# Performance work log

Hardware: AMD Instinct MI355X
Metric: run time of the kernel (lower is better)

Reference implementation:

```python
import jax, jax.numpy as jnp
import numpy as np

N = 100000
F_IN = 128
HID = 128
NCLS = 40
NEG_SLOPE = 0.2
BN_EPS = 1e-5


def setup_inputs() -> dict:
    key = jax.random.key(0)
    ks = jax.random.split(key, 16)
    x = jax.random.normal(ks[0], (N, F_IN), dtype=jnp.float32)
    # self-loop-free random edges: dst = (src + 1 + r) % N
    E = 1600000
    src = jax.random.randint(ks[1], (E,), 0, N)
    off = jax.random.randint(ks[2], (E,), 1, N)
    dst = (src + off) % N
    edge_index = jnp.stack([src, dst]).astype(jnp.int64)

    def glorot(k, shape):
        fan = shape[0] + shape[-1]
        s = jnp.sqrt(6.0 / fan)
        return jax.random.uniform(k, shape, jnp.float32, -s, s)

    params = {
        'W1': glorot(ks[3], (F_IN, HID)),
        'as1': glorot(ks[4], (HID,)), 'ad1': glorot(ks[5], (HID,)),
        'b1': jnp.zeros((HID,), jnp.float32),
        'g1': jnp.ones((HID,), jnp.float32), 'beta1': jnp.zeros((HID,), jnp.float32),
        'W2': glorot(ks[6], (HID, HID)),
        'as2': glorot(ks[7], (HID,)), 'ad2': glorot(ks[8], (HID,)),
        'b2': jnp.zeros((HID,), jnp.float32),
        'g2': jnp.ones((HID,), jnp.float32), 'beta2': jnp.zeros((HID,), jnp.float32),
        'Wc': glorot(ks[9], (HID, NCLS)),
        'bc': jnp.zeros((NCLS,), jnp.float32),
    }
    return {'x': x, 'edge_index': edge_index, **params}


def _gat_conv(h_in, src, dst, W, a_src, a_dst, bias):
    # heads=1, concat=False -> single head, mean over heads is identity
    h = h_in @ W                               # [N, C]
    alpha_s = h @ a_src                        # [N]
    alpha_d = h @ a_dst                        # [N]
    alpha = alpha_s[src] + alpha_d[dst]        # [E] edge score
    alpha = jax.nn.leaky_relu(alpha, NEG_SLOPE)
    # segment softmax over destination node neighborhoods
    m = jax.ops.segment_max(alpha, dst, num_segments=N)
    e = jnp.exp(alpha - m[dst])
    s = jax.ops.segment_sum(e, dst, num_segments=N)
    alpha = e / s[dst]
    msg = h[src] * alpha[:, None]              # [E, C]
    out = jax.ops.segment_sum(msg, dst, num_segments=N)
    return out + bias


def _batchnorm(x, gamma, beta):
    mu = jnp.mean(x, axis=0)
    var = jnp.mean(jnp.square(x - mu), axis=0)  # biased, as torch BN training
    return (x - mu) * jax.lax.rsqrt(var + BN_EPS) * gamma + beta


def reference(x, edge_index, W1, as1, ad1, b1, g1, beta1,
              W2, as2, ad2, b2, g2, beta2, Wc, bc):
    src, dst = edge_index[0], edge_index[1]
    # add self loops (input edges are guaranteed self-loop-free)
    loop = jnp.arange(N, dtype=src.dtype)
    src = jnp.concatenate([src, loop])
    dst = jnp.concatenate([dst, loop])

    h = _gat_conv(x, src, dst, W1, as1, ad1, b1)
    h = jax.nn.relu(_batchnorm(h, g1, beta1))
    h = _gat_conv(h, src, dst, W2, as2, ad2, b2)
    h = jax.nn.relu(_batchnorm(h, g2, beta2))
    return h @ Wc + bc
```

## Files before the change

### kernel.cpp

```cpp
#include <hip/hip_runtime.h>
#include <math.h>


#define CDIM 128
#define NCLS_ 40
#define NEG_SLOPE_ 0.2f
#define BN_EPS_ 1e-5f
#define BRNG 256
#define BCAP 6144
#define EPB 16

using short8  = __attribute__((ext_vector_type(8))) short;
using short4v = __attribute__((ext_vector_type(4))) short;
using f32x4   = __attribute__((ext_vector_type(4))) float;

static __device__ __forceinline__ float lrelu(float a) {
    return a > 0.f ? a : NEG_SLOPE_ * a;
}
static __device__ __forceinline__ short f2bf(float f) {
    unsigned u = __float_as_uint(f);
    u += 0x7fffu + ((u >> 16) & 1u);
    return (short)(u >> 16);
}
static __device__ __forceinline__ float bf_lo(unsigned u) { return __uint_as_float(u << 16); }
static __device__ __forceinline__ float bf_hi(unsigned u) { return __uint_as_float(u & 0xffff0000u); }

__global__ void k_setup(int* bcur, float* bnsum, int NB, int n, int E, int* offs,
                        const float* __restrict__ W1, const float* __restrict__ W2,
                        const float* __restrict__ Wc,
                        short* __restrict__ Wt1, short* __restrict__ Wt2,
                        short* __restrict__ Wtc) {
    int i = blockIdx.x * blockDim.x + threadIdx.x;
    if (i < NB) bcur[i] = 0;
    if (i < 512) bnsum[i] = 0.f;
    if (i == 0) offs[n] = E + n;
    if (i < 128 * 128) {
        int k = i >> 7, nn = i & 127;
        Wt1[nn * 128 + k] = f2bf(W1[i]);
        Wt2[nn * 128 + k] = f2bf(W2[i]);
    }
    if (i < 48 * 128) {
        int nn = i >> 7, k = i & 127;
        Wtc[i] = (nn < NCLS_) ? f2bf(Wc[k * NCLS_ + nn]) : (short)0;
    }
}

__global__ __launch_bounds__(256) void k_binA(
    const int* __restrict__ src, const int* __restrict__ dst, int E,
    int* __restrict__ bcur, uint2* __restrict__ bucket, int NB)
{
    __shared__ int hist[400];
    __shared__ int base[400];
    int t = threadIdx.x;
    long e0 = (long)blockIdx.x * (256 * EPB) + t;

    for (int i = t; i < NB; i += 256) hist[i] = 0;
    __syncthreads();

    int sv[EPB], dv[EPB];
    #pragma unroll
    for (int i = 0; i < EPB; i++) {
        long e = e0 + (long)i * 256;
        if (e < E) {
            sv[i] = src[e]; dv[i] = dst[e];
            atomicAdd(&hist[dv[i] >> 8], 1);
        } else dv[i] = -1;
    }
    __syncthreads();

    for (int i = t; i < NB; i += 256) {
        int h = hist[i];
        base[i] = (h > 0) ? atomicAdd(&bcur[i], h) : 0;
    }
    __syncthreads();
    for (int i = t; i < NB; i += 256) hist[i] = 0;
    __syncthreads();

    #pragma unroll
    for (int i = 0; i < EPB; i++) {
        if (dv[i] >= 0) {
            int b = dv[i] >> 8;
            int pos = base[b] + atomicAdd(&hist[b], 1);
            if (pos < BCAP)
                bucket[(size_t)b * BCAP + pos] =
                    make_uint2((unsigned)sv[i], (unsigned)dv[i]);
        }
    }
}

__global__ __launch_bounds__(256) void k_fillB(
    const uint2* __restrict__ bucket, const int* __restrict__ bcur,
    int n, int NB, int* __restrict__ offs, int* __restrict__ csr)
{
    __shared__ int hist[256];
    __shared__ int scanb[256];
    __shared__ int cur[256];
    __shared__ int buf[BCAP + BRNG];
    int b = blockIdx.x, t = threadIdx.x;
    int node0 = b << 8;
    int nodesIn = min(BRNG, n - node0);
    int cnt = min(bcur[b], BCAP);
    const uint2* mybkt = bucket + (size_t)b * BCAP;

    int part = 0;
    for (int j = t; j < b; j += 256) part += min(bcur[j], BCAP);
    scanb[t] = part; __syncthreads();
    for (int s2 = 128; s2 > 0; s2 >>= 1) {
        if (t < s2) scanb[t] += scanb[t + s2];
        __syncthreads();
    }
    int base = scanb[0] + node0;
    __syncthreads();

    hist[t] = 0; __syncthreads();
    for (int e2 = t; e2 < cnt; e2 += 256)
        atomicAdd(&hist[mybkt[e2].y & 255], 1);
    __syncthreads();

    int v = hist[t] + ((t < nodesIn) ? 1 : 0);
    scanb[t] = v; __syncthreads();
    for (int d = 1; d < 256; d <<= 1) {
        int x2 = (t >= d) ? scanb[t - d] : 0;
        __syncthreads();
        scanb[t] += x2;
        __syncthreads();
    }
    int lo = scanb[t] - v;
    if (t < nodesIn) {
        offs[node0 + t] = base + lo;
        buf[lo] = node0 + t;
        cur[t] = lo + 1;
    }
    __syncthreads();

    for (int e2 = t; e2 < cnt; e2 += 256) {
        uint2 ed = mybkt[e2];
        int pos = atomicAdd(&cur[ed.y & 255], 1);
        buf[pos] = (int)ed.x;
    }
    __syncthreads();

    int tot = cnt + nodesIn;
    for (int j2 = t; j2 < tot; j2 += 256) csr[base + j2] = buf[j2];
}

__global__ __launch_bounds__(256) void k_gemm_mfma(
    const float* __restrict__ Xf, const unsigned* __restrict__ Xb,
    const short* __restrict__ Wt,
    const float* __restrict__ bnsum, const float* __restrict__ gamma,
    const float* __restrict__ beta, float invn,
    const float* __restrict__ av_s, const float* __restrict__ av_d,
    short* __restrict__ Hb, float* __restrict__ alpha_s, float* __restrict__ alpha_d,
    int n, int fuse)
{
    __shared__ short As[64 * 128];
    __shared__ short Bs[128 * 128];
    __shared__ float part_s[4][64];
    __shared__ float part_d[4][64];
    int t = threadIdx.x;
    int row0 = blockIdx.x * 64;

    for (int j = 0; j < 8; j++) {
        int idx = j * 256 + t;
        int nn = idx >> 4, cc = idx & 15;
        *(short8*)(Bs + nn * 128 + cc * 8) = *(const short8*)(Wt + nn * 128 + cc * 8);
    }
    float4 sc4 = make_float4(1.f, 1.f, 1.f, 1.f);
    float4 sh4 = make_float4(0.f, 0.f, 0.f, 0.f);
    if (fuse) {
        int cb = (t & 31) * 4;
        float4 s0 = *(const float4*)(bnsum + cb);
        float4 s1 = *(const float4*)(bnsum + 128 + cb);
        float4 gm = *(const float4*)(gamma + cb);
        float4 bt = *(const float4*)(beta + cb);
        float mean, var;
        mean = s0.x * invn; var = fmaxf(s1.x * invn - mean * mean, 0.f);
        sc4.x = gm.x * rsqrtf(var + BN_EPS_); sh4.x = bt.x - mean * sc4.x;
        mean = s0.y * invn; var = fmaxf(s1.y * invn - mean * mean, 0.f);
        sc4.y = gm.y * rsqrtf(var + BN_EPS_); sh4.y = bt.y - mean * sc4.y;
        mean = s0.z * invn; var = fmaxf(s1.z * invn - mean * mean, 0.f);
        sc4.z = gm.z * rsqrtf(var + BN_EPS_); sh4.z = bt.z - mean * sc4.z;
        mean = s0.w * invn; var = fmaxf(s1.w * invn - mean * mean, 0.f);
        sc4.w = gm.w * rsqrtf(var + BN_EPS_); sh4.w = bt.w - mean * sc4.w;
    }
    for (int j = 0; j < 8; j++) {
        int idx = j * 256 + t;
        int r = idx >> 5, k4 = idx & 31;
        int gr = row0 + r;
        float4 xv = make_float4(0.f, 0.f, 0.f, 0.f);
        if (fuse) {
            if (gr < n) {
                uint2 u = *(const uint2*)(Xb + (size_t)gr * 64 + k4 * 2);
                xv.x = bf_lo(u.x); xv.y = bf_hi(u.x);
                xv.z = bf_lo(u.y); xv.w = bf_hi(u.y);
            }
            xv.x = fmaxf(fmaf(xv.x, sc4.x, sh4.x), 0.f);
            xv.y = fmaxf(fmaf(xv.y, sc4.y, sh4.y), 0.f);
            xv.z = fmaxf(fmaf(xv.z, sc4.z, sh4.z), 0.f);
            xv.w = fmaxf(fmaf(xv.w, sc4.w, sh4.w), 0.f);
        } else {
            if (gr < n) xv = *(const float4*)(Xf + (size_t)gr * CDIM + k4 * 4);
        }
        short4v o;
        o.x = f2bf(xv.x); o.y = f2bf(xv.y); o.z = f2bf(xv.z); o.w = f2bf(xv.w);
        *(short4v*)(As + r * 128 + k4 * 4) = o;
    }
    __syncthreads();

    int w = t >> 6, lane = t & 63, q = lane >> 4, c = lane & 15;
    f32x4 zero = {0.f, 0.f, 0.f, 0.f};
    f32x4 acc[4][2];
    for (int i = 0; i < 4; i++) { acc[i][0] = zero; acc[i][1] = zero; }

    for (int ks = 0; ks < 4; ks++) {
        int k0 = ks * 32 + q * 8;
        short8 a0 = *(short8*)(As + (c) * 128 + k0);
        short8 a1 = *(short8*)(As + (16 + c) * 128 + k0);
        short8 a2 = *(short8*)(As + (32 + c) * 128 + k0);
        short8 a3 = *(short8*)(As + (48 + c) * 128 + k0);
        short8 b0 = *(short8*)(Bs + (w * 32 + c) * 128 + k0);
        short8 b1 = *(short8*)(Bs + (w * 32 + 16 + c) * 128 + k0);
        acc[0][0] = __builtin_amdgcn_mfma_f32_16x16x32_bf16(a0, b0, acc[0][0], 0, 0, 0);
        acc[1][0] = __builtin_amdgcn_mfma_f32_16x16x32_bf16(a1, b0, acc[1][0], 0, 0, 0);
        acc[2][0] = __builtin_amdgcn_mfma_f32_16x16x32_bf16(a2, b0, acc[2][0], 0, 0, 0);
        acc[3][0] = __builtin_amdgcn_mfma_f32_16x16x32_bf16(a3, b0, acc[3][0], 0, 0, 0);
        acc[0][1] = __builtin_amdgcn_mfma_f32_16x16x32_bf16(a0, b1, acc[0][1], 0, 0, 0);
        acc[1][1] = __builtin_amdgcn_mfma_f32_16x16x32_bf16(a1, b1, acc[1][1], 0, 0, 0);
        acc[2][1] = __builtin_amdgcn_mfma_f32_16x16x32_bf16(a2, b1, acc[2][1], 0, 0, 0);
        acc[3][1] = __builtin_amdgcn_mfma_f32_16x16x32_bf16(a3, b1, acc[3][1], 0, 0, 0);
    }

    float as0 = av_s[w * 32 + c],      as1 = av_s[w * 32 + 16 + c];
    float ad0 = av_d[w * 32 + c],      ad1 = av_d[w * 32 + 16 + c];
    #pragma unroll
    for (int mt = 0; mt < 4; mt++) {
        #pragma unroll
        for (int r = 0; r < 4; r++) {
            float v0 = acc[mt][0][r], v1 = acc[mt][1][r];
            float ps = v0 * as0 + v1 * as1;
            float pd = v0 * ad0 + v1 * ad1;
            #pragma unroll
            for (int off = 1; off < 16; off <<= 1) {
                ps += __shfl_xor(ps, off);
                pd += __shfl_xor(pd, off);
            }
            if (c == 0) {
                part_s[w][mt * 16 + q * 4 + r] = ps;
                part_d[w][mt * 16 + q * 4 + r] = pd;
            }
        }
    }
    __syncthreads();

    short* Hs = As;
    #pragma unroll
    for (int mt = 0; mt < 4; mt++)
        #pragma unroll
        for (int nt = 0; nt < 2; nt++)
            #pragma unroll
            for (int r = 0; r < 4; r++)
                Hs[(mt * 16 + q * 4 + r) * 128 + w * 32 + nt * 16 + c] = f2bf(acc[mt][nt][r]);

    if (t < 64) {
        int row = row0 + t;
        if (row < n) {
            alpha_s[row] = part_s[0][t] + part_s[1][t] + part_s[2][t] + part_s[3][t];
            alpha_d[row] = part_d[0][t] + part_d[1][t] + part_d[2][t] + part_d[3][t];
        }
    }
    __syncthreads();

    for (int j = 0; j < 4; j++) {
        int idx = j * 256 + t;
        int r = idx >> 4, cc = idx & 15;
        int gr = row0 + r;
        if (gr < n)
            *(short8*)(Hb + (size_t)gr * 128 + cc * 8) = *(short8*)(Hs + r * 128 + cc * 8);
    }
}

__global__ __launch_bounds__(256) void k_agg(
    const uint2* __restrict__ Hb2, const int* __restrict__ offs,
    const int* __restrict__ csr, const float* __restrict__ alpha_s,
    const float* __restrict__ alpha_d, const float* __restrict__ bias,
    uint2* __restrict__ Ob, int n)
{
    int i = blockIdx.x * 8 + (threadIdx.x >> 5);
    int l = threadIdx.x & 31;
    if (i >= n) return;
    int o0 = offs[i], o1 = offs[i + 1];
    float adi = alpha_d[i];
    int hoff = (threadIdx.x & 32) << 2;

    float m = -1e30f, se = 0.f;
    float a0 = 0.f, a1 = 0.f, a2 = 0.f, a3 = 0.f;

    for (int c0 = o0; c0 < o1; c0 += 32) {
        int j = c0 + l;
        int cnt = min(32, o1 - c0);
        int sj = (j < o1) ? csr[j] : 0;
        float a = (j < o1) ? lrelu(alpha_s[sj] + adi) : -1e30f;

        float cm = a;
        #pragma unroll
        for (int o = 16; o > 0; o >>= 1) cm = fmaxf(cm, __shfl_xor(cm, o));
        if (cm > m) {
            float r = __expf(m - cm);
            se *= r; a0 *= r; a1 *= r; a2 *= r; a3 *= r;
            m = cm;
        }
        float wl = (j < o1) ? __expf(a - m) : 0.f;
        se += wl;
        int wli = (int)__float_as_uint(wl);

        int cntmax = max(cnt, __shfl_xor(cnt, 32));
        for (int b = 0; b < cntmax; b += 4) {
            uint2 u[4]; float wv[4];
            #pragma unroll
            for (int q2 = 0; q2 < 4; q2++) {
                int el = min(b + q2, 31);
                int addr = hoff + (el << 2);
                int s = __builtin_amdgcn_ds_bpermute(addr, sj);
                wv[q2] = __uint_as_float((unsigned)__builtin_amdgcn_ds_bpermute(addr, wli));
                u[q2] = Hb2[(size_t)(unsigned)s * 32 + l];
            }
            #pragma unroll
            for (int q2 = 0; q2 < 4; q2++) {
                a0 = fmaf(wv[q2], bf_lo(u[q2].x), a0);
                a1 = fmaf(wv[q2], bf_hi(u[q2].x), a1);
                a2 = fmaf(wv[q2], bf_lo(u[q2].y), a2);
                a3 = fmaf(wv[q2], bf_hi(u[q2].y), a3);
            }
        }
    }

    #pragma unroll
    for (int o = 16; o > 0; o >>= 1) se += __shfl_xor(se, o);
    float inv = 1.f / se;
    float4 b4 = *(const float4*)(bias + l * 4);
    float r0 = fmaf(a0, inv, b4.x);
    float r1 = fmaf(a1, inv, b4.y);
    float r2 = fmaf(a2, inv, b4.z);
    float r3 = fmaf(a3, inv, b4.w);
    uint2 pk;
    pk.x = ((unsigned)(unsigned short)f2bf(r1) << 16) | (unsigned)(unsigned short)f2bf(r0);
    pk.y = ((unsigned)(unsigned short)f2bf(r3) << 16) | (unsigned)(unsigned short)f2bf(r2);
    Ob[(size_t)i * 32 + l] = pk;
}

__global__ void k_bnstats(const unsigned* __restrict__ Hb, int n, float* __restrict__ sums) {
    __shared__ float red[4][64][4];
    int w = threadIdx.x & 63;
    int g = threadIdx.x >> 6;
    float slo = 0.f, shi = 0.f, qlo = 0.f, qhi = 0.f;
    for (int r = blockIdx.x * 4 + g; r < n; r += gridDim.x * 4) {
        unsigned u = Hb[(size_t)r * 64 + w];
        float lo = bf_lo(u), hi = bf_hi(u);
        slo += lo; shi += hi; qlo += lo * lo; qhi += hi * hi;
    }
    red[g][w][0] = slo; red[g][w][1] = shi; red[g][w][2] = qlo; red[g][w][3] = qhi;
    __syncthreads();
    if (threadIdx.x < 64) {
        int w2 = threadIdx.x;
        float s0 = 0.f, s1 = 0.f, s2 = 0.f, s3 = 0.f;
        for (int gg = 0; gg < 4; gg++) {
            s0 += red[gg][w2][0]; s1 += red[gg][w2][1];
            s2 += red[gg][w2][2]; s3 += red[gg][w2][3];
        }
        atomicAdd(&sums[2 * w2], s0);
        atomicAdd(&sums[2 * w2 + 1], s1);
        atomicAdd(&sums[128 + 2 * w2], s2);
        atomicAdd(&sums[128 + 2 * w2 + 1], s3);
    }
}

__global__ __launch_bounds__(256) void k_cls(
    const unsigned* __restrict__ G, const short* __restrict__ Wtc,
    const float* __restrict__ bc, const float* __restrict__ bnsum,
    const float* __restrict__ gamma, const float* __restrict__ beta, float invn,
    float* __restrict__ out, int n)
{
    __shared__ short As[64 * 128];
    __shared__ short Bs[48 * 128];
    int t = threadIdx.x;
    int row0 = blockIdx.x * 64;

    for (int j = 0; j < 3; j++) {
        int idx = j * 256 + t;
        *(short8*)(Bs + idx * 8) = *(const short8*)(Wtc + idx * 8);
    }
    float4 sc4, sh4;
    {
        int cb = (t & 31) * 4;
        float4 s0 = *(const float4*)(bnsum + cb);
        float4 s1 = *(const float4*)(bnsum + 128 + cb);
        float4 gm = *(const float4*)(gamma + cb);
        float4 bt = *(const float4*)(beta + cb);
        float mean, var;
        mean = s0.x * invn; var = fmaxf(s1.x * invn - mean * mean, 0.f);
        sc4.x = gm.x * rsqrtf(var + BN_EPS_); sh4.x = bt.x - mean * sc4.x;
        mean = s0.y * invn; var = fmaxf(s1.y * invn - mean * mean, 0.f);
        sc4.y = gm.y * rsqrtf(var + BN_EPS_); sh4.y = bt.y - mean * sc4.y;
        mean = s0.z * invn; var = fmaxf(s1.z * invn - mean * mean, 0.f);
        sc4.z = gm.z * rsqrtf(var + BN_EPS_); sh4.z = bt.z - mean * sc4.z;
        mean = s0.w * invn; var = fmaxf(s1.w * invn - mean * mean, 0.f);
        sc4.w = gm.w * rsqrtf(var + BN_EPS_); sh4.w = bt.w - mean * sc4.w;
    }
    for (int j = 0; j < 8; j++) {
        int idx = j * 256 + t;
        int r = idx >> 5, k4 = idx & 31;
        int gr = row0 + r;
        float4 xv = make_float4(0.f, 0.f, 0.f, 0.f);
        if (gr < n) {
            uint2 u = *(const uint2*)(G + (size_t)gr * 64 + k4 * 2);
            xv.x = bf_lo(u.x); xv.y = bf_hi(u.x);
            xv.z = bf_lo(u.y); xv.w = bf_hi(u.y);
        }
        xv.x = fmaxf(fmaf(xv.x, sc4.x, sh4.x), 0.f);
        xv.y = fmaxf(fmaf(xv.y, sc4.y, sh4.y), 0.f);
        xv.z = fmaxf(fmaf(xv.z, sc4.z, sh4.z), 0.f);
        xv.w = fmaxf(fmaf(xv.w, sc4.w, sh4.w), 0.f);
        short4v o;
        o.x = f2bf(xv.x); o.y = f2bf(xv.y); o.z = f2bf(xv.z); o.w = f2bf(xv.w);
        *(short4v*)(As + r * 128 + k4 * 4) = o;
    }
    __syncthreads();

    int w = t >> 6, lane = t & 63, q = lane >> 4, c = lane & 15;
    f32x4 zero = {0.f, 0.f, 0.f, 0.f};
    f32x4 acc[3] = {zero, zero, zero};
    for (int ks = 0; ks < 4; ks++) {
        int k0 = ks * 32 + q * 8;
        short8 a  = *(short8*)(As + (w * 16 + c) * 128 + k0);
        short8 b0 = *(short8*)(Bs + (c) * 128 + k0);
        short8 b1 = *(short8*)(Bs + (16 + c) * 128 + k0);
        short8 b2 = *(short8*)(Bs + (32 + c) * 128 + k0);
        acc[0] = __builtin_amdgcn_mfma_f32_16x16x32_bf16(a, b0, acc[0], 0, 0, 0);
        acc[1] = __builtin_amdgcn_mfma_f32_16x16x32_bf16(a, b1, acc[1], 0, 0, 0);
        acc[2] = __builtin_amdgcn_mfma_f32_16x16x32_bf16(a, b2, acc[2], 0, 0, 0);
    }
    float bc0 = bc[c], bc1 = bc[16 + c], bc2 = (c < 8) ? bc[32 + c] : 0.f;
    #pragma unroll
    for (int r = 0; r < 4; r++) {
        int row = row0 + w * 16 + q * 4 + r;
        if (row < n) {
            out[(size_t)row * NCLS_ + c]      = acc[0][r] + bc0;
            out[(size_t)row * NCLS_ + 16 + c] = acc[1][r] + bc1;
            if (c < 8) out[(size_t)row * NCLS_ + 32 + c] = acc[2][r] + bc2;
        }
    }
}

extern "C" void kernel_launch(void* const* d_in, const int* in_sizes, int n_in,
                              void* d_out, int out_size, void* d_ws, size_t ws_size,
                              hipStream_t stream)
{
    const float* x   = (const float*)d_in[0];
    const int*   ei  = (const int*)d_in[1];
    const float* W1  = (const float*)d_in[2];
    const float* as1 = (const float*)d_in[3];
    const float* ad1 = (const float*)d_in[4];
    const float* b1  = (const float*)d_in[5];
    const float* g1  = (const float*)d_in[6];
    const float* be1 = (const float*)d_in[7];
    const float* W2  = (const float*)d_in[8];
    const float* as2 = (const float*)d_in[9];
    const float* ad2 = (const float*)d_in[10];
    const float* b2  = (const float*)d_in[11];
    const float* g2  = (const float*)d_in[12];
    const float* be2 = (const float*)d_in[13];
    const float* Wc  = (const float*)d_in[14];
    const float* bc  = (const float*)d_in[15];
    float* out = (float*)d_out;

    int n = in_sizes[0] / CDIM;
    int E = in_sizes[1] / 2;
    const int* src = ei;
    const int* dst = ei + E;
    float invn = 1.f / (float)n;
    int NB = (n + BRNG - 1) / BRNG;

    char* p = (char*)d_ws;
    auto alloc = [&p](size_t bytes) { char* q = p; p += (bytes + 63) & ~(size_t)63; return q; };
    short*    Hb      = (short*)alloc((size_t)n * CDIM * sizeof(short));
    unsigned* bufB    = (unsigned*)alloc((size_t)n * 64 * sizeof(unsigned));
    float*    alpha_s = (float*)alloc((size_t)n * sizeof(float));
    float*    alpha_d = (float*)alloc((size_t)n * sizeof(float));
    float*    bnsum   = (float*)alloc(512 * sizeof(float));
    short*    Wt1     = (short*)alloc(128 * 128 * sizeof(short));
    short*    Wt2     = (short*)alloc(128 * 128 * sizeof(short));
    short*    Wtc     = (short*)alloc(48 * 128 * sizeof(short));
    int*      bcurs   = (int*)alloc((size_t)NB * sizeof(int));
    int*      offs    = (int*)alloc((size_t)(n + 1) * sizeof(int));
    uint2*    bucket  = (uint2*)alloc((size_t)NB * BCAP * sizeof(uint2));
    int*      csr     = (int*)alloc((size_t)(E + n) * sizeof(int));

    k_setup<<<dim3(64), dim3(256), 0, stream>>>(bcurs, bnsum, NB, n, E, offs,
                                                W1, W2, Wc, Wt1, Wt2, Wtc);
    k_binA<<<dim3((E + 4095) / 4096), dim3(256), 0, stream>>>(src, dst, E, bcurs, bucket, NB);
    k_fillB<<<dim3(NB), dim3(256), 0, stream>>>(bucket, bcurs, n, NB, offs, csr);

    dim3 ggrid((n + 63) / 64);
    dim3 wgrid((n + 7) / 8);

    k_gemm_mfma<<<ggrid, 256, 0, stream>>>(x, nullptr, Wt1, nullptr, nullptr, nullptr,
                                           invn, as1, ad1, Hb, alpha_s, alpha_d, n, 0);
    k_agg<<<wgrid, 256, 0, stream>>>((const uint2*)Hb, offs, csr, alpha_s, alpha_d,
                                     b1, (uint2*)bufB, n);
    k_bnstats<<<dim3(256), dim3(256), 0, stream>>>(bufB, n, bnsum);

    k_gemm_mfma<<<ggrid, 256, 0, stream>>>(nullptr, bufB, Wt2, bnsum, g1, be1,
                                           invn, as2, ad2, Hb, alpha_s, alpha_d, n, 1);
    k_agg<<<wgrid, 256, 0, stream>>>((const uint2*)Hb, offs, csr, alpha_s, alpha_d,
                                     b2, (uint2*)bufB, n);
    k_bnstats<<<dim3(256), dim3(256), 0, stream>>>(bufB, n, bnsum + 256);

    k_cls<<<ggrid, 256, 0, stream>>>(bufB, Wtc, bc, bnsum + 256, g2, be2, invn, out, n);
}
```

Before: 451.0 us.

## Store GAT features as fp16 and aggregate with packed half2 FMA, one node per wave

The GEMM now writes the projected features as fp16 instead of bf16. The aggregation kernel gives one 64-lane wave to each node, with 2 channels per lane. It broadcasts neighbour indices and weights with readlane instead of ds_bpermute and accumulates with packed __hfma2 in fp16. The intent is to halve the FMA instruction count, drop the LDS permutes and simplify the gather. The cost is fp16 accumulation, which risks precision loss and overflow on nodes with many neighbours. Each gathered row is also now a 256-byte load issued by a single wave, and every readlane is a scalar dependency in the loop.

```diff
diff --git a/kernel.cpp b/kernel.cpp
--- a/kernel.cpp
+++ b/kernel.cpp
@@ -1,4 +1,5 @@
 #include <hip/hip_runtime.h>
+#include <hip/hip_fp16.h>
 #include <math.h>
 
 
@@ -24,6 +25,8 @@
 }
 static __device__ __forceinline__ float bf_lo(unsigned u) { return __uint_as_float(u << 16); }
 static __device__ __forceinline__ float bf_hi(unsigned u) { return __uint_as_float(u & 0xffff0000u); }
+static __device__ __forceinline__ __half2 u2h2(unsigned u) { return __builtin_bit_cast(__half2, u); }
+static __device__ __forceinline__ unsigned h22u(__half2 h) { return __builtin_bit_cast(unsigned, h); }
 
 __global__ void k_setup(int* bcur, float* bnsum, int NB, int n, int E, int* offs,
                         const float* __restrict__ W1, const float* __restrict__ W2,
@@ -150,7 +153,7 @@
     const float* __restrict__ bnsum, const float* __restrict__ gamma,
     const float* __restrict__ beta, float invn,
     const float* __restrict__ av_s, const float* __restrict__ av_d,
-    short* __restrict__ Hb, float* __restrict__ alpha_s, float* __restrict__ alpha_d,
+    short* __restrict__ Hh, float* __restrict__ alpha_s, float* __restrict__ alpha_d,
     int n, int fuse)
 {
     __shared__ short As[64 * 128];
@@ -259,7 +262,8 @@
         for (int nt = 0; nt < 2; nt++)
             #pragma unroll
             for (int r = 0; r < 4; r++)
-                Hs[(mt * 16 + q * 4 + r) * 128 + w * 32 + nt * 16 + c] = f2bf(acc[mt][nt][r]);
+                Hs[(mt * 16 + q * 4 + r) * 128 + w * 32 + nt * 16 + c] =
+                    (short)__half_as_ushort(__float2half_rn(acc[mt][nt][r]));
 
     if (t < 64) {
         int row = row0 + t;
@@ -275,77 +279,71 @@
         int r = idx >> 4, cc = idx & 15;
         int gr = row0 + r;
         if (gr < n)
-            *(short8*)(Hb + (size_t)gr * 128 + cc * 8) = *(short8*)(Hs + r * 128 + cc * 8);
+            *(short8*)(Hh + (size_t)gr * 128 + cc * 8) = *(short8*)(Hs + r * 128 + cc * 8);
     }
 }
 
 __global__ __launch_bounds__(256) void k_agg(
-    const uint2* __restrict__ Hb2, const int* __restrict__ offs,
+    const unsigned* __restrict__ Hh, const int* __restrict__ offs,
     const int* __restrict__ csr, const float* __restrict__ alpha_s,
     const float* __restrict__ alpha_d, const float* __restrict__ bias,
-    uint2* __restrict__ Ob, int n)
+    unsigned* __restrict__ Ob, int n)
 {
-    int i = blockIdx.x * 8 + (threadIdx.x >> 5);
-    int l = threadIdx.x & 31;
+    int i = blockIdx.x * 4 + (threadIdx.x >> 6);
+    int lane = threadIdx.x & 63;
     if (i >= n) return;
     int o0 = offs[i], o1 = offs[i + 1];
     float adi = alpha_d[i];
-    int hoff = (threadIdx.x & 32) << 2;
-
-    float m = -1e30f, se = 0.f;
-    float a0 = 0.f, a1 = 0.f, a2 = 0.f, a3 = 0.f;
-
-    for (int c0 = o0; c0 < o1; c0 += 32) {
-        int j = c0 + l;
-        int cnt = min(32, o1 - c0);
+
+    float m = -1e30f;
+    float se = 0.f;
+    __half2 acc2 = __floats2half2_rn(0.f, 0.f);
+
+    for (int c0 = o0; c0 < o1; c0 += 64) {
+        int j = c0 + lane;
+        int cnt = min(64, o1 - c0);
         int sj = (j < o1) ? csr[j] : 0;
         float a = (j < o1) ? lrelu(alpha_s[sj] + adi) : -1e30f;
 
         float cm = a;
         #pragma unroll
-        for (int o = 16; o > 0; o >>= 1) cm = fmaxf(cm, __shfl_xor(cm, o));
+        for (int o = 32; o > 0; o >>= 1) cm = fmaxf(cm, __shfl_xor(cm, o));
         if (cm > m) {
             float r = __expf(m - cm);
-            se *= r; a0 *= r; a1 *= r; a2 *= r; a3 *= r;
+            se *= r;
+            acc2 = __hmul2(acc2, __float2half2_rn(r));
             m = cm;
         }
         float wl = (j < o1) ? __expf(a - m) : 0.f;
         se += wl;
-        int wli = (int)__float_as_uint(wl);
-
-        int cntmax = max(cnt, __shfl_xor(cnt, 32));
-        for (int b = 0; b < cntmax; b += 4) {
-            uint2 u[4]; float wv[4];
+        int wli = (int)h22u(__float2half2_rn(wl));
+
+        for (int b = 0; b < cnt; b += 8) {
+            unsigned u[8]; int wb[8];
             #pragma unroll
-            for (int q2 = 0; q2 < 4; q2++) {
-                int el = min(b + q2, 31);
-                int addr = hoff + (el << 2);
-                int s = __builtin_amdgcn_ds_bpermute(addr, sj);
-                wv[q2] = __uint_as_float((unsigned)__builtin_amdgcn_ds_bpermute(addr, wli));
-                u[q2] = Hb2[(size_t)(unsigned)s * 32 + l];
+            for (int q2 = 0; q2 < 8; q2++) {
+                int el = min(b + q2, 63);
+                int s = __builtin_amdgcn_readlane(sj, el);
+                wb[q2] = __builtin_amdgcn_readlane(wli, el);
+                u[q2] = Hh[(size_t)(unsigned)s * 64 + lane];
             }
             #pragma unroll
-            for (int q2 = 0; q2 < 4; q2++) {
-                a0 = fmaf(wv[q2], bf_lo(u[q2].x), a0);
-                a1 = fmaf(wv[q2], bf_hi(u[q2].x), a1);
-                a2 = fmaf(wv[q2], bf_lo(u[q2].y), a2);
-                a3 = fmaf(wv[q2], bf_hi(u[q2].y), a3);
+            for (int q2 = 0; q2 < 8; q2++) {
+                acc2 = __hfma2(u2h2(u[q2]), u2h2((unsigned)wb[q2]), acc2);
             }
         }
     }
 
     #pragma unroll
-    for (int o = 16; o > 0; o >>= 1) se += __shfl_xor(se, o);
+    for (int o = 32; o > 0; o >>= 1) se += __shfl_xor(se, o);
     float inv = 1.f / se;
-    float4 b4 = *(const float4*)(bias + l * 4);
-    float r0 = fmaf(a0, inv, b4.x);
-    float r1 = fmaf(a1, inv, b4.y);
-    float r2 = fmaf(a2, inv, b4.z);
-    float r3 = fmaf(a3, inv, b4.w);
-    uint2 pk;
-    pk.x = ((unsigned)(unsigned short)f2bf(r1) << 16) | (unsigned)(unsigned short)f2bf(r0);
-    pk.y = ((unsigned)(unsigned short)f2bf(r3) << 16) | (unsigned)(unsigned short)f2bf(r2);
-    Ob[(size_t)i * 32 + l] = pk;
+    float2 af = __half22float2(acc2);
+    float2 b2 = *(const float2*)(bias + lane * 2);
+    float rx = fmaf(af.x, inv, b2.x);
+    float ry = fmaf(af.y, inv, b2.y);
+    unsigned pack = ((unsigned)(unsigned short)f2bf(ry) << 16) |
+                    (unsigned)(unsigned short)f2bf(rx);
+    Ob[(size_t)i * 64 + lane] = pack;
 }
 
 __global__ void k_bnstats(const unsigned* __restrict__ Hb, int n, float* __restrict__ sums) {
@@ -482,7 +480,7 @@
 
     char* p = (char*)d_ws;
     auto alloc = [&p](size_t bytes) { char* q = p; p += (bytes + 63) & ~(size_t)63; return q; };
-    short*    Hb      = (short*)alloc((size_t)n * CDIM * sizeof(short));
+    short*    Hh      = (short*)alloc((size_t)n * CDIM * sizeof(short));
     unsigned* bufB    = (unsigned*)alloc((size_t)n * 64 * sizeof(unsigned));
     float*    alpha_s = (float*)alloc((size_t)n * sizeof(float));
     float*    alpha_d = (float*)alloc((size_t)n * sizeof(float));
@@ -501,18 +499,18 @@
     k_fillB<<<dim3(NB), dim3(256), 0, stream>>>(bucket, bcurs, n, NB, offs, csr);
 
     dim3 ggrid((n + 63) / 64);
-    dim3 wgrid((n + 7) / 8);
+    dim3 wgrid((n + 3) / 4);
 
     k_gemm_mfma<<<ggrid, 256, 0, stream>>>(x, nullptr, Wt1, nullptr, nullptr, nullptr,
-                                           invn, as1, ad1, Hb, alpha_s, alpha_d, n, 0);
-    k_agg<<<wgrid, 256, 0, stream>>>((const uint2*)Hb, offs, csr, alpha_s, alpha_d,
-                                     b1, (uint2*)bufB, n);
+                                           invn, as1, ad1, Hh, alpha_s, alpha_d, n, 0);
+    k_agg<<<wgrid, 256, 0, stream>>>((const unsigned*)Hh, offs, csr, alpha_s, alpha_d,
+                                     b1, bufB, n);
     k_bnstats<<<dim3(256), dim3(256), 0, stream>>>(bufB, n, bnsum);
 
     k_gemm_mfma<<<ggrid, 256, 0, stream>>>(nullptr, bufB, Wt2, bnsum, g1, be1,
-                                           invn, as2, ad2, Hb, alpha_s, alpha_d, n, 1);
-    k_agg<<<wgrid, 256, 0, stream>>>((const uint2*)Hb, offs, csr, alpha_s, alpha_d,
-                                     b2, (uint2*)bufB, n);
+                                           invn, as2, ad2, Hh, alpha_s, alpha_d, n, 1);
+    k_agg<<<wgrid, 256, 0, stream>>>((const unsigned*)Hh, offs, csr, alpha_s, alpha_d,
+                                     b2, bufB, n);
     k_bnstats<<<dim3(256), dim3(256), 0, stream>>>(bufB, n, bnsum + 256);
 
     k_cls<<<ggrid, 256, 0, stream>>>(bufB, Wtc, bc, bnsum + 256, g2, be2, invn, out, n);
```

After: 443.1 us. About the same (-1.8%).
